# Optimization experiments

Measured on AMD Instinct MI355X. Metric: run time of the kernel, lower is better.

## Reference

```python
import jax, jax.numpy as jnp
import numpy as np

EPS = 1e-5

def _block(x, W, b, g, be):
    # Linear -> LayerNorm -> ReLU, fused elementwise chain
    h = x @ W + b
    mu = jnp.mean(h, axis=-1, keepdims=True)
    var = jnp.mean(jnp.square(h - mu), axis=-1, keepdims=True)
    hn = (h - mu) * jax.lax.rsqrt(var + EPS) * g + be
    return jnp.maximum(hn, 0.0)

def setup_inputs() -> dict:
    key = jax.random.key(0)
    ks = jax.random.split(key, 6)
    B, D_IN, H, D_OUT = 262144, 48, 256, 12
    s_in = 1.0 / np.sqrt(D_IN)
    s_h = 1.0 / np.sqrt(H)
    return {
        "x": jax.random.normal(ks[0], (B, D_IN), jnp.float32),
        "W1": jax.random.normal(ks[1], (D_IN, H), jnp.float32) * s_in,
        "b1": jnp.zeros((H,), jnp.float32),
        "g1": jnp.ones((H,), jnp.float32),
        "be1": jnp.zeros((H,), jnp.float32),
        "W2": jax.random.normal(ks[2], (H, H), jnp.float32) * s_h,
        "b2": jnp.zeros((H,), jnp.float32),
        "g2": jnp.ones((H,), jnp.float32),
        "be2": jnp.zeros((H,), jnp.float32),
        "W3": jax.random.normal(ks[3], (H, H), jnp.float32) * s_h,
        "b3": jnp.zeros((H,), jnp.float32),
        "g3": jnp.ones((H,), jnp.float32),
        "be3": jnp.zeros((H,), jnp.float32),
        "Wm": jax.random.normal(ks[4], (H, D_OUT), jnp.float32) * s_h,
        "bm": jnp.zeros((D_OUT,), jnp.float32),
    }

def reference(x, W1, b1, g1, be1, W2, b2, g2, be2, W3, b3, g3, be3, Wm, bm):
    h = _block(x, W1, b1, g1, be1)
    h = _block(h, W2, b2, g2, be2)
    h = _block(h, W3, b3, g3, be3)
    return jnp.tanh(h @ Wm + bm)
```

## Files before the change

kernel.cpp:

```cpp
#include <hip/hip_runtime.h>
#include <hip/hip_bf16.h>

#define BATCH 262144
#define DIN 48
#define HDIM 256
#define DOUT 12
#define EPSV 1e-5f

#define ROWS_PER_BLOCK 128
#define NBLK (BATCH / ROWS_PER_BLOCK)

typedef __attribute__((ext_vector_type(4))) float f32x4;
typedef __attribute__((ext_vector_type(2))) float f32x2;
typedef __attribute__((ext_vector_type(8))) short bf16x8;

union FragU { bf16x8 v; unsigned u[4]; };

#define W1F_OFF 0
#define W2F_OFF 16384
#define W3F_OFF 81920
#define WMF_OFF 147456
#define WS_ELEMS 151552

#define WAITV(n) asm volatile("s_waitcnt vmcnt(" #n ")" ::: "memory")

__device__ __forceinline__ unsigned short f2b(float f) {
    union { float f; unsigned u; } v; v.f = f;
    unsigned r = (v.u + 0x7fffu + ((v.u >> 16) & 1u)) >> 16;
    return (unsigned short)r;
}

__device__ __forceinline__ unsigned packbf(float a, float b) {
    float2 t; t.x = a; t.y = b;
    __hip_bfloat162 h = __float22bfloat162_rn(t);
    union { __hip_bfloat162 h; unsigned u; } c; c.h = h;
    return c.u;
}

__device__ __forceinline__ float fast_tanh(float x) {
    const float t = __expf(2.0f * x);
    return fmaf(-2.0f, __builtin_amdgcn_rcpf(t + 1.0f), 1.0f);
}

__global__ void conv_w_kernel(const float* __restrict__ W1, const float* __restrict__ b1,
                              const float* __restrict__ W2, const float* __restrict__ W3,
                              const float* __restrict__ Wm,
                              unsigned short* __restrict__ ws) {
    int i = blockIdx.x * 256 + threadIdx.x;
    if (i >= WS_ELEMS) return;
    float v;
    if (i < W2F_OFF) {
        const int j = i & 7, l = (i >> 3) & 63, t = (i >> 9) & 15, s = i >> 13;
        const int n = 16 * t + (l & 15), k = 32 * s + 8 * (l >> 4) + j;
        v = (k < DIN) ? W1[k * HDIM + n] : (k == DIN ? b1[n] : 0.0f);
    } else if (i < W3F_OFF) {
        const int i2 = i - W2F_OFF;
        const int j = i2 & 7, l = (i2 >> 3) & 63, t = (i2 >> 9) & 15, s = i2 >> 13;
        const int n = 16 * t + (l & 15);
        const int k = 32 * s + ((j >= 4) ? 16 : 0) + 4 * (l >> 4) + (j & 3);
        v = W2[k * HDIM + n];
    } else if (i < WMF_OFF) {
        const int i3 = i - W3F_OFF;
        const int j = i3 & 7, l = (i3 >> 3) & 63, t = (i3 >> 9) & 15, s = i3 >> 13;
        const int n = 16 * t + (l & 15);
        const int k = 32 * s + ((j >= 4) ? 16 : 0) + 4 * (l >> 4) + (j & 3);
        v = W3[k * HDIM + n];
    } else {
        const int i4 = i - WMF_OFF;
        const int j = i4 & 7, l = (i4 >> 3) & 63, ks = i4 >> 9;
        const int n = l & 15;
        const int k = 32 * ks + ((j >= 4) ? 16 : 0) + 4 * (l >> 4) + (j & 3);
        v = (n < DOUT) ? Wm[k * DOUT + n] : 0.0f;
    }
    ws[i] = f2b(v);
}

__device__ __forceinline__ void gll16(const void* g, void* l) {
    __builtin_amdgcn_global_load_lds(
        (const __attribute__((address_space(1))) unsigned int*)g,
        (__attribute__((address_space(3))) unsigned int*)l, 16, 0, 0);
}

__device__ __forceinline__ void stage_slab(const unsigned short* __restrict__ src,
                                           unsigned short* dst, int tid) {
    const char* g = (const char*)src + tid * 16;
    char* l = (char*)dst + tid * 16;
    #pragma unroll
    for (int c = 0; c < 4; c++)
        gll16(g + c * 4096, l + c * 4096);
}

__device__ __forceinline__ void compute_slab(
    f32x4 (&acc)[2][16], const FragU& b0, const FragU& b1,
    const unsigned short* sb, int lane)
{
    __builtin_amdgcn_s_setprio(1);
    #pragma unroll
    for (int t = 0; t < 16; t++) {
        const bf16x8 A = *(const bf16x8*)&sb[(t * 64 + lane) * 8];
        acc[0][t] = __builtin_amdgcn_mfma_f32_16x16x32_bf16(A, b0.v, acc[0][t], 0, 0, 0);
        acc[1][t] = __builtin_amdgcn_mfma_f32_16x16x32_bf16(A, b1.v, acc[1][t], 0, 0, 0);
    }
    __builtin_amdgcn_s_setprio(0);
}

#define SV2(v, a, b) __builtin_shufflevector(v, v, a, b)

__device__ __forceinline__ void build_frags(
    const f32x4 (&acc)[2][16], FragU (&bfo)[2][8],
    const float* __restrict__ gt, const float* __restrict__ bt, int lane)
{
    const int q4 = (lane >> 4) * 4;
    #pragma unroll
    for (int rt = 0; rt < 2; rt++) {
        f32x2 s2 = {0.f, 0.f}, p2 = {0.f, 0.f};
        #pragma unroll
        for (int t = 0; t < 16; t++) {
            const f32x2 a = SV2(acc[rt][t], 0, 1);
            const f32x2 b = SV2(acc[rt][t], 2, 3);
            s2 += a; s2 += b;
            p2 += a * a; p2 += b * b;
        }
        float ss = s2[0] + s2[1];
        float qq = p2[0] + p2[1];
        ss += __shfl_xor(ss, 16); ss += __shfl_xor(ss, 32);
        qq += __shfl_xor(qq, 16); qq += __shfl_xor(qq, 32);
        const float mu = ss * (1.0f / 256.0f);
        const float rs = __builtin_amdgcn_rsqf(
            fmaxf(qq * (1.0f / 256.0f) - mu * mu, 0.0f) + EPSV);
        const float nb = -mu * rs;
        const f32x2 rs2 = {rs, rs}, nb2 = {nb, nb}, z2 = {0.f, 0.f};
        #pragma unroll
        for (int ks = 0; ks < 8; ks++) {
            const f32x4 g0 = *(const f32x4*)&gt[32 * ks + q4];
            const f32x4 e0 = *(const f32x4*)&bt[32 * ks + q4];
            const f32x4 g1 = *(const f32x4*)&gt[32 * ks + 16 + q4];
            const f32x4 e1 = *(const f32x4*)&bt[32 * ks + 16 + q4];
            const f32x2 v00 = SV2(acc[rt][2 * ks], 0, 1);
            const f32x2 v01 = SV2(acc[rt][2 * ks], 2, 3);
            const f32x2 v10 = SV2(acc[rt][2 * ks + 1], 0, 1);
            const f32x2 v11 = SV2(acc[rt][2 * ks + 1], 2, 3);
            const f32x2 w00 = __builtin_elementwise_max(
                (v00 * rs2 + nb2) * SV2(g0, 0, 1) + SV2(e0, 0, 1), z2);
            const f32x2 w01 = __builtin_elementwise_max(
                (v01 * rs2 + nb2) * SV2(g0, 2, 3) + SV2(e0, 2, 3), z2);
            const f32x2 w10 = __builtin_elementwise_max(
                (v10 * rs2 + nb2) * SV2(g1, 0, 1) + SV2(e1, 0, 1), z2);
            const f32x2 w11 = __builtin_elementwise_max(
                (v11 * rs2 + nb2) * SV2(g1, 2, 3) + SV2(e1, 2, 3), z2);
            bfo[rt][ks].u[0] = packbf(w00[0], w00[1]);
            bfo[rt][ks].u[1] = packbf(w01[0], w01[1]);
            bfo[rt][ks].u[2] = packbf(w10[0], w10[1]);
            bfo[rt][ks].u[3] = packbf(w11[0], w11[1]);
        }
    }
}

__device__ __forceinline__ void zero_acc(f32x4 (&acc)[2][16]) {
    #pragma unroll
    for (int rt = 0; rt < 2; rt++)
        #pragma unroll
        for (int t = 0; t < 16; t++)
            acc[rt][t] = (f32x4){0.f, 0.f, 0.f, 0.f};
}

__device__ __forceinline__ void init_acc_bias(f32x4 (&acc)[2][16],
                                              const float* __restrict__ bt, int q) {
    #pragma unroll
    for (int t = 0; t < 16; t++) {
        const f32x4 b = *(const f32x4*)&bt[16 * t + 4 * q];
        acc[0][t] = b;
        acc[1][t] = b;
    }
}

__global__ __launch_bounds__(256, 2) void fused_mlp(
    const float* __restrict__ x,
    const float* __restrict__ g1, const float* __restrict__ be1,
    const float* __restrict__ b2, const float* __restrict__ g2, const float* __restrict__ be2,
    const float* __restrict__ b3, const float* __restrict__ g3, const float* __restrict__ be3,
    const float* __restrict__ bm,
    const unsigned short* __restrict__ ws,
    float* __restrict__ out)
{
    __shared__ unsigned short buf[4][8192];
    __shared__ float gtab[3][256];
    __shared__ float betab[3][256];
    __shared__ float btab[2][256];
    __shared__ float bmt[16];
    __shared__ float ostage[4][384];

    const int tid = threadIdx.x;
    const int wv = tid >> 6, lane = tid & 63;
    const int l15 = lane & 15, q = lane >> 4;
    const int wrow0 = blockIdx.x * ROWS_PER_BLOCK + wv * 32;

    const unsigned short* w1f = ws + W1F_OFF;
    const unsigned short* w2f = ws + W2F_OFF;
    const unsigned short* w3f = ws + W3F_OFF;
    const unsigned short* wmf = ws + WMF_OFF;

    stage_slab(w1f, &buf[0][0], tid);
    stage_slab(w1f + 8192, &buf[1][0], tid);

    {
        const int n = tid;
        gtab[0][n] = g1[n];  betab[0][n] = be1[n];
        gtab[1][n] = g2[n];  betab[1][n] = be2[n];
        gtab[2][n] = g3[n];  betab[2][n] = be3[n];
        btab[0][n] = b2[n];
        btab[1][n] = b3[n];
        if (tid < 16) bmt[tid] = (tid < DOUT) ? bm[tid] : 0.f;
    }
    FragU bf[2][8];
    #pragma unroll
    for (int rt = 0; rt < 2; rt++) {
        const float* xr = x + (size_t)(wrow0 + rt * 16 + l15) * DIN;
        const float4 f0 = *(const float4*)(xr + q * 8);
        const float4 f1 = *(const float4*)(xr + q * 8 + 4);
        bf[rt][0].u[0] = packbf(f0.x, f0.y); bf[rt][0].u[1] = packbf(f0.z, f0.w);
        bf[rt][0].u[2] = packbf(f1.x, f1.y); bf[rt][0].u[3] = packbf(f1.z, f1.w);
        if (q < 2) {
            const float4 f2 = *(const float4*)(xr + 32 + q * 8);
            const float4 f3 = *(const float4*)(xr + 36 + q * 8);
            bf[rt][1].u[0] = packbf(f2.x, f2.y); bf[rt][1].u[1] = packbf(f2.z, f2.w);
            bf[rt][1].u[2] = packbf(f3.x, f3.y); bf[rt][1].u[3] = packbf(f3.z, f3.w);
        } else if (q == 2) {
            bf[rt][1].u[0] = 0x00003F80u;
            bf[rt][1].u[1] = 0u; bf[rt][1].u[2] = 0u; bf[rt][1].u[3] = 0u;
        } else {
            bf[rt][1].u[0] = 0u; bf[rt][1].u[1] = 0u;
            bf[rt][1].u[2] = 0u; bf[rt][1].u[3] = 0u;
        }
    }
    asm volatile("s_waitcnt lgkmcnt(0)" ::: "memory");

    f32x4 acc[2][16];


    zero_acc(acc);
    #pragma unroll
    for (int s = 0; s < 2; s++) {
        stage_slab(w2f + s * 8192, &buf[(s + 2) & 3][0], tid);
        WAITV(8);
        __builtin_amdgcn_s_barrier();
        __builtin_amdgcn_sched_barrier(0);
        compute_slab(acc, bf[0][s], bf[1][s], &buf[s][0], lane);
    }
    build_frags(acc, bf, &gtab[0][0], &betab[0][0], lane);

    init_acc_bias(acc, &btab[0][0], q);
    #pragma unroll
    for (int s = 0; s < 8; s++) {
        const unsigned short* nsrc = (s < 6) ? (w2f + (s + 2) * 8192)
                                             : (w3f + (s - 6) * 8192);
        stage_slab(nsrc, &buf[(s + 4) & 3][0], tid);
        WAITV(8);
        __builtin_amdgcn_s_barrier();
        __builtin_amdgcn_sched_barrier(0);
        compute_slab(acc, bf[0][s], bf[1][s], &buf[(s + 2) & 3][0], lane);
    }
    build_frags(acc, bf, &gtab[1][0], &betab[1][0], lane);

    init_acc_bias(acc, &btab[1][0], q);
    #pragma unroll
    for (int s = 0; s < 8; s++) {
        if (s < 6) stage_slab(w3f + (s + 2) * 8192, &buf[(s + 12) & 3][0], tid);
        if (s < 6)      { WAITV(8); }
        else if (s == 6){ WAITV(4); }
        else            { WAITV(0); }
        __builtin_amdgcn_s_barrier();
        __builtin_amdgcn_sched_barrier(0);
        compute_slab(acc, bf[0][s], bf[1][s], &buf[(s + 10) & 3][0], lane);
    }
    build_frags(acc, bf, &gtab[2][0], &betab[2][0], lane);

    f32x4 facc[2];
    {
        const f32x4 bm4 = *(const f32x4*)&bmt[4 * q];
        facc[0] = bm4;
        facc[1] = bm4;
    }
    #pragma unroll
    for (int ks = 0; ks < 8; ks++) {
        const bf16x8 A = *(const bf16x8*)&wmf[(ks * 64 + lane) * 8];
        facc[0] = __builtin_amdgcn_mfma_f32_16x16x32_bf16(A, bf[0][ks].v, facc[0], 0, 0, 0);
        facc[1] = __builtin_amdgcn_mfma_f32_16x16x32_bf16(A, bf[1][ks].v, facc[1], 0, 0, 0);
    }
    if (q < 3) {
        #pragma unroll
        for (int rt = 0; rt < 2; rt++) {
            float4 o;
            o.x = fast_tanh(facc[rt][0]);
            o.y = fast_tanh(facc[rt][1]);
            o.z = fast_tanh(facc[rt][2]);
            o.w = fast_tanh(facc[rt][3]);
            *(float4*)&ostage[wv][(rt * 16 + l15) * 12 + q * 4] = o;
        }
    }
    float4* og = (float4*)(out + (size_t)wrow0 * DOUT);
    const float4* ov = (const float4*)&ostage[wv][0];
    og[lane] = ov[lane];
    if (lane < 32) og[64 + lane] = ov[64 + lane];
}

extern "C" void kernel_launch(void* const* d_in, const int* in_sizes, int n_in,
                              void* d_out, int out_size, void* d_ws, size_t ws_size,
                              hipStream_t stream)
{
    const float* x   = (const float*)d_in[0];
    const float* W1  = (const float*)d_in[1];
    const float* b1  = (const float*)d_in[2];
    const float* g1  = (const float*)d_in[3];
    const float* be1 = (const float*)d_in[4];
    const float* W2  = (const float*)d_in[5];
    const float* b2  = (const float*)d_in[6];
    const float* g2  = (const float*)d_in[7];
    const float* be2 = (const float*)d_in[8];
    const float* W3  = (const float*)d_in[9];
    const float* b3  = (const float*)d_in[10];
    const float* g3  = (const float*)d_in[11];
    const float* be3 = (const float*)d_in[12];
    const float* Wm  = (const float*)d_in[13];
    const float* bm  = (const float*)d_in[14];
    unsigned short* ws = (unsigned short*)d_ws;
    float* out = (float*)d_out;

    conv_w_kernel<<<(WS_ELEMS + 255) / 256, 256, 0, stream>>>(W1, b1, W2, W3, Wm, ws);
    fused_mlp<<<NBLK, 256, 0, stream>>>(x, g1, be1, b2, g2, be2,
                                        b3, g3, be3, bm, ws, out);
}
```

Measured before the change: 100.6 us.

## Read weight fragments directly from global memory instead of LDS-staged pipeline

Removes the shared-memory staging ring, the async global-to-LDS slab loads, and the per-slab barriers. Each wave now loads its bf16 weight fragments straight from global memory (relying on L2/L1 caching) and reads the LayerNorm gamma/beta and bias vectors from global as well. The output tile is written directly from registers rather than staged through LDS for coalesced stores. This drops barrier and LDS overhead and frees LDS, but every wave now fetches the whole weight set from cache with no shared reuse, and the output stores are less coalesced.

After: 336.5 us. 235% more time.

```diff
diff --git a/kernel.cpp b/kernel.cpp
--- a/kernel.cpp
+++ b/kernel.cpp
@@ -21,8 +21,6 @@
 #define W3F_OFF 81920
 #define WMF_OFF 147456
 #define WS_ELEMS 151552
-
-#define WAITV(n) asm volatile("s_waitcnt vmcnt(" #n ")" ::: "memory")
 
 __device__ __forceinline__ unsigned short f2b(float f) {
     union { float f; unsigned u; } v; v.f = f;
@@ -75,33 +73,20 @@
     ws[i] = f2b(v);
 }
 
-__device__ __forceinline__ void gll16(const void* g, void* l) {
-    __builtin_amdgcn_global_load_lds(
-        (const __attribute__((address_space(1))) unsigned int*)g,
-        (__attribute__((address_space(3))) unsigned int*)l, 16, 0, 0);
-}
-
-__device__ __forceinline__ void stage_slab(const unsigned short* __restrict__ src,
-                                           unsigned short* dst, int tid) {
-    const char* g = (const char*)src + tid * 16;
-    char* l = (char*)dst + tid * 16;
-    #pragma unroll
-    for (int c = 0; c < 4; c++)
-        gll16(g + c * 4096, l + c * 4096);
-}
-
-__device__ __forceinline__ void compute_slab(
-    f32x4 (&acc)[2][16], const FragU& b0, const FragU& b1,
-    const unsigned short* sb, int lane)
-{
-    __builtin_amdgcn_s_setprio(1);
-    #pragma unroll
-    for (int t = 0; t < 16; t++) {
-        const bf16x8 A = *(const bf16x8*)&sb[(t * 64 + lane) * 8];
-        acc[0][t] = __builtin_amdgcn_mfma_f32_16x16x32_bf16(A, b0.v, acc[0][t], 0, 0, 0);
-        acc[1][t] = __builtin_amdgcn_mfma_f32_16x16x32_bf16(A, b1.v, acc[1][t], 0, 0, 0);
-    }
-    __builtin_amdgcn_s_setprio(0);
+template<int KS>
+__device__ __forceinline__ void mm_layer_g(
+    f32x4 (&acc)[2][16], const FragU (&bf)[2][8],
+    const unsigned short* __restrict__ wf, int lane)
+{
+    #pragma unroll
+    for (int s = 0; s < KS; s++) {
+        #pragma unroll
+        for (int t = 0; t < 16; t++) {
+            const bf16x8 A = *(const bf16x8*)&wf[((s * 16 + t) * 64 + lane) * 8];
+            acc[0][t] = __builtin_amdgcn_mfma_f32_16x16x32_bf16(A, bf[0][s].v, acc[0][t], 0, 0, 0);
+            acc[1][t] = __builtin_amdgcn_mfma_f32_16x16x32_bf16(A, bf[1][s].v, acc[1][t], 0, 0, 0);
+        }
+    }
 }
 
 #define SV2(v, a, b) __builtin_shufflevector(v, v, a, b)
@@ -183,13 +168,6 @@
     const unsigned short* __restrict__ ws,
     float* __restrict__ out)
 {
-    __shared__ unsigned short buf[4][8192];
-    __shared__ float gtab[3][256];
-    __shared__ float betab[3][256];
-    __shared__ float btab[2][256];
-    __shared__ float bmt[16];
-    __shared__ float ostage[4][384];
-
     const int tid = threadIdx.x;
     const int wv = tid >> 6, lane = tid & 63;
     const int l15 = lane & 15, q = lane >> 4;
@@ -200,18 +178,6 @@
     const unsigned short* w3f = ws + W3F_OFF;
     const unsigned short* wmf = ws + WMF_OFF;
 
-    stage_slab(w1f, &buf[0][0], tid);
-    stage_slab(w1f + 8192, &buf[1][0], tid);
-
-    {
-        const int n = tid;
-        gtab[0][n] = g1[n];  betab[0][n] = be1[n];
-        gtab[1][n] = g2[n];  betab[1][n] = be2[n];
-        gtab[2][n] = g3[n];  betab[2][n] = be3[n];
-        btab[0][n] = b2[n];
-        btab[1][n] = b3[n];
-        if (tid < 16) bmt[tid] = (tid < DOUT) ? bm[tid] : 0.f;
-    }
     FragU bf[2][8];
     #pragma unroll
     for (int rt = 0; rt < 2; rt++) {
@@ -233,51 +199,25 @@
             bf[rt][1].u[2] = 0u; bf[rt][1].u[3] = 0u;
         }
     }
-    asm volatile("s_waitcnt lgkmcnt(0)" ::: "memory");
 
     f32x4 acc[2][16];
 
-
     zero_acc(acc);
-    #pragma unroll
-    for (int s = 0; s < 2; s++) {
-        stage_slab(w2f + s * 8192, &buf[(s + 2) & 3][0], tid);
-        WAITV(8);
-        __builtin_amdgcn_s_barrier();
-        __builtin_amdgcn_sched_barrier(0);
-        compute_slab(acc, bf[0][s], bf[1][s], &buf[s][0], lane);
-    }
-    build_frags(acc, bf, &gtab[0][0], &betab[0][0], lane);
-
-    init_acc_bias(acc, &btab[0][0], q);
-    #pragma unroll
-    for (int s = 0; s < 8; s++) {
-        const unsigned short* nsrc = (s < 6) ? (w2f + (s + 2) * 8192)
-                                             : (w3f + (s - 6) * 8192);
-        stage_slab(nsrc, &buf[(s + 4) & 3][0], tid);
-        WAITV(8);
-        __builtin_amdgcn_s_barrier();
-        __builtin_amdgcn_sched_barrier(0);
-        compute_slab(acc, bf[0][s], bf[1][s], &buf[(s + 2) & 3][0], lane);
-    }
-    build_frags(acc, bf, &gtab[1][0], &betab[1][0], lane);
-
-    init_acc_bias(acc, &btab[1][0], q);
-    #pragma unroll
-    for (int s = 0; s < 8; s++) {
-        if (s < 6) stage_slab(w3f + (s + 2) * 8192, &buf[(s + 12) & 3][0], tid);
-        if (s < 6)      { WAITV(8); }
-        else if (s == 6){ WAITV(4); }
-        else            { WAITV(0); }
-        __builtin_amdgcn_s_barrier();
-        __builtin_amdgcn_sched_barrier(0);
-        compute_slab(acc, bf[0][s], bf[1][s], &buf[(s + 10) & 3][0], lane);
-    }
-    build_frags(acc, bf, &gtab[2][0], &betab[2][0], lane);
+    mm_layer_g<2>(acc, bf, w1f, lane);
+    build_frags(acc, bf, g1, be1, lane);
+
+    init_acc_bias(acc, b2, q);
+    mm_layer_g<8>(acc, bf, w2f, lane);
+    build_frags(acc, bf, g2, be2, lane);
+
+    init_acc_bias(acc, b3, q);
+    mm_layer_g<8>(acc, bf, w3f, lane);
+    build_frags(acc, bf, g3, be3, lane);
 
     f32x4 facc[2];
     {
-        const f32x4 bm4 = *(const f32x4*)&bmt[4 * q];
+        f32x4 bm4 = {0.f, 0.f, 0.f, 0.f};
+        if (q < 3) bm4 = *(const f32x4*)&bm[4 * q];
         facc[0] = bm4;
         facc[1] = bm4;
     }
@@ -295,13 +235,9 @@
             o.y = fast_tanh(facc[rt][1]);
             o.z = fast_tanh(facc[rt][2]);
             o.w = fast_tanh(facc[rt][3]);
-            *(float4*)&ostage[wv][(rt * 16 + l15) * 12 + q * 4] = o;
-        }
-    }
-    float4* og = (float4*)(out + (size_t)wrow0 * DOUT);
-    const float4* ov = (const float4*)&ostage[wv][0];
-    og[lane] = ov[lane];
-    if (lane < 32) og[64 + lane] = ov[64 + lane];
+            *(float4*)&out[(size_t)(wrow0 + rt * 16 + l15) * DOUT + q * 4] = o;
+        }
+    }
 }
 
 extern "C" void kernel_launch(void* const* d_in, const int* in_sizes, int n_in,
```
